# Kernel optimization log

Measured on AMD Instinct MI355X. Metric: run time of the kernel, lower is better.

The kernel has to match this reference:

```python
import jax, jax.numpy as jnp
import numpy as np

B, SQ, HIDDEN = 2, 2048, 2048
HEADS, GROUPS, KVC = 16, 4, 128
HPG = HEADS // GROUPS          # heads per group
LAYER_INDEX = 1
SCALE = KVC ** -0.5            # attention_softmax_scale_power = 0.5


def setup_inputs() -> dict:
    key = jax.random.key(0)
    k1, k2, k3, k4 = jax.random.split(key, 4)
    return {
        "x": jax.random.normal(k1, (B, SQ, HIDDEN), jnp.float32),
        "w_q": jax.random.normal(k2, (HIDDEN, HEADS * KVC), jnp.float32) * 0.02,
        "w_kv": jax.random.normal(k3, (HIDDEN, 2 * GROUPS * KVC), jnp.float32) * 0.02,
        "w_dense": jax.random.normal(k4, (HEADS * KVC, HIDDEN), jnp.float32) * 0.02,
    }


def reference(x, w_q, w_kv, w_dense):
    b, sq, _ = x.shape
    sk = sq
    # QKV projections
    q = jnp.einsum("bsh,he->bse", x, w_q).reshape(b, sq, GROUPS, HPG, KVC)
    kv = jnp.einsum("bsh,he->bse", x, w_kv)
    k, v = jnp.split(kv, 2, axis=-1)
    k = k.reshape(b, sk, GROUPS, KVC)
    v = v.reshape(b, sk, GROUPS, KVC)
    # scaled QK^T with the per-layer scale trick: alpha = scale/L in input
    # dtype, then cast to fp32 and multiply by L (as in _attn_fused)
    scores = jnp.einsum("bqgpd,bkgd->bgqpk", q, k) * (SCALE / LAYER_INDEX)
    scores = scores.astype(jnp.float32) * LAYER_INDEX
    # causal mask: mask = ~triu(ones, diagonal=1) -> keep where q_idx >= k_idx
    causal = (jnp.arange(sq)[:, None] >= jnp.arange(sk)[None, :])
    scores = jnp.where(causal[None, None, :, None, :], scores, -jnp.inf)
    probs = jax.nn.softmax(scores, axis=-1).astype(x.dtype)
    # dropout p = 0.0 -> no-op
    ctx = jnp.einsum("bgqpk,bkgd->bqgpd", probs, v).reshape(b, sq, HEADS * KVC)
    return jnp.einsum("bse,eh->bsh", ctx, w_dense)
```

## Files before the change

### kernel.cpp

```cpp
#include <hip/hip_runtime.h>
#include <hip/hip_bf16.h>


typedef __attribute__((ext_vector_type(4))) float f32x4;
typedef __attribute__((ext_vector_type(8))) short bf16x8;
typedef __attribute__((ext_vector_type(4))) short bf16x4;

__device__ __forceinline__ unsigned short f2bf(float f) {
    unsigned u = __builtin_bit_cast(unsigned, f);
    unsigned r = u + 0x7fffu + ((u >> 16) & 1u);
    return (unsigned short)(r >> 16);
}

__device__ __forceinline__ unsigned cvtpk_bf16(float lo, float hi) {
    unsigned r;
    asm("v_cvt_pk_bf16_f32 %0, %1, %2" : "=v"(r) : "v"(lo), "v"(hi));
    return r;
}

__device__ __forceinline__ void gl_lds16(const void* g, void* l) {
    __builtin_amdgcn_global_load_lds(
        (const __attribute__((address_space(1))) unsigned int*)g,
        (__attribute__((address_space(3))) unsigned int*)l, 16, 0, 0);
}

__global__ __launch_bounds__(256)
void xcvt_kernel(const float* __restrict__ in, unsigned short* __restrict__ out)
{
    size_t i = ((size_t)blockIdx.x * 256 + threadIdx.x) * 8;
    float4 a = *reinterpret_cast<const float4*>(&in[i]);
    float4 b = *reinterpret_cast<const float4*>(&in[i + 4]);
    bf16x8 o = { (short)f2bf(a.x), (short)f2bf(a.y),
                 (short)f2bf(a.z), (short)f2bf(a.w),
                 (short)f2bf(b.x), (short)f2bf(b.y),
                 (short)f2bf(b.z), (short)f2bf(b.w) };
    *reinterpret_cast<bf16x8*>(&out[i]) = o;
}

__global__ __launch_bounds__(256)
void wtrans_kernel(const float* __restrict__ in, unsigned short* __restrict__ out,
                   int K, int N)
{
    __shared__ unsigned short T[64][72];
    const int n0 = blockIdx.x * 64, k0 = blockIdx.y * 64;
    const int tid = threadIdx.x;
#pragma unroll
    for (int i = 0; i < 4; ++i) {
        int f = tid + i * 256;
        int r = f >> 4;
        int c4 = (f & 15) * 4;
        float4 v = *reinterpret_cast<const float4*>(&in[(size_t)(k0 + r) * N + n0 + c4]);
        bf16x4 pk = { (short)f2bf(v.x), (short)f2bf(v.y),
                      (short)f2bf(v.z), (short)f2bf(v.w) };
        *reinterpret_cast<bf16x4*>(&T[r][c4]) = pk;
    }
    __syncthreads();
#pragma unroll
    for (int i = 0; i < 2; ++i) {
        int f = tid + i * 256;
        int nn = f >> 3;
        int s8 = (f & 7) * 8;
        bf16x8 o;
#pragma unroll
        for (int j = 0; j < 8; ++j) o[j] = T[s8 + j][nn];
        *reinterpret_cast<bf16x8*>(&out[(size_t)(n0 + nn) * K + k0 + s8]) = o;
    }
}

template<bool SPLIT_QKV>
__global__ __launch_bounds__(256)
void gemm_bt_kernel(const unsigned short* __restrict__ A,
                    const unsigned short* __restrict__ BT,
                    void* __restrict__ C0v, void* __restrict__ C1v,
                    int M, int N, int K)
{
    __shared__ __align__(16) unsigned short Alds[2][128 * 64];
    __shared__ __align__(16) unsigned short Blds[2][128 * 64];

    const int tid = threadIdx.x;
    const int lane = tid & 63;
    const int wid = tid >> 6;
    const int wr = wid >> 1, wc = wid & 1;
    const int m0 = blockIdx.y * 128;
    const int n0 = blockIdx.x * 128;
    const int l16 = lane & 15, lg = lane >> 4;

    f32x4 acc[4][4];
#pragma unroll
    for (int m = 0; m < 4; ++m)
#pragma unroll
        for (int n = 0; n < 4; ++n) acc[m][n] = (f32x4){0.f, 0.f, 0.f, 0.f};

    auto stage = [&](int kt, int bi) {
#pragma unroll
        for (int i = 0; i < 4; ++i) {
            int row = i * 32 + (tid >> 3);
            int cb = ((tid & 7) * 16) ^ ((row & 7) << 4);
            gl_lds16((const char*)A + ((size_t)(m0 + row) * K + kt) * 2 + cb,
                     (char*)(&Alds[bi][0]) + i * 4096 + wid * 1024);
            gl_lds16((const char*)BT + ((size_t)(n0 + row) * K + kt) * 2 + cb,
                     (char*)(&Blds[bi][0]) + i * 4096 + wid * 1024);
        }
    };

    const int NK = K / 64;
    stage(0, 0);
    int cur = 0;

    for (int kti = 0; kti < NK; ++kti) {
        if (kti + 1 < NK) {
            stage((kti + 1) * 64, cur ^ 1);
            asm volatile("s_waitcnt vmcnt(8)" ::: "memory");
        } else {
            asm volatile("s_waitcnt vmcnt(0)" ::: "memory");
        }
        __builtin_amdgcn_s_barrier();

        const char* Ab = (const char*)(&Alds[cur][0]);
        const char* Bb = (const char*)(&Blds[cur][0]);

        bf16x8 af[2][4], bf[2][4];
#pragma unroll
        for (int kd = 0; kd < 2; ++kd) {
#pragma unroll
            for (int m = 0; m < 4; ++m) {
                int row = wr * 64 + m * 16 + l16;
                af[kd][m] = *reinterpret_cast<const bf16x8*>(
                    Ab + row * 128 + ((kd * 64 + lg * 16) ^ ((row & 7) << 4)));
            }
#pragma unroll
            for (int n = 0; n < 4; ++n) {
                int row = wc * 64 + n * 16 + l16;
                bf[kd][n] = *reinterpret_cast<const bf16x8*>(
                    Bb + row * 128 + ((kd * 64 + lg * 16) ^ ((row & 7) << 4)));
            }
        }
#pragma unroll
        for (int kd = 0; kd < 2; ++kd)
#pragma unroll
            for (int m = 0; m < 4; ++m)
#pragma unroll
                for (int n = 0; n < 4; ++n)
                    acc[m][n] = __builtin_amdgcn_mfma_f32_16x16x32_bf16(
                        af[kd][m], bf[kd][n], acc[m][n], 0, 0, 0);

        __builtin_amdgcn_s_barrier();
        cur ^= 1;
    }

#pragma unroll
    for (int m = 0; m < 4; ++m) {
#pragma unroll
        for (int n = 0; n < 4; ++n) {
#pragma unroll
            for (int r = 0; r < 4; ++r) {
                int row = m0 + wr * 64 + m * 16 + lg * 4 + r;
                int col = n0 + wc * 64 + n * 16 + l16;
                float val = acc[m][n][r];
                if constexpr (SPLIT_QKV) {
                    if (n0 < 2048)
                        ((unsigned short*)C0v)[(size_t)row * 2048 + col] =
                            f2bf(val * 0.12751879523209208f);
                    else
                        ((unsigned short*)C1v)[(size_t)row * 1024 + (col - 2048)] = f2bf(val);
                } else {
                    ((float*)C0v)[(size_t)row * N + col] = val;
                }
            }
        }
    }
}

__global__ __launch_bounds__(256)
void vtrans_kernel(const unsigned short* __restrict__ kv,
                   unsigned short* __restrict__ vt)
{
    __shared__ unsigned short T[64][140];
    const int bg = blockIdx.y;
    const int b = bg >> 2, g = bg & 3;
    const int s0 = blockIdx.x * 64;
    const int tid = threadIdx.x;

#pragma unroll
    for (int i = 0; i < 4; ++i) {
        int f = tid + i * 256;
        int sl = f >> 4;
        int d0 = (f & 15) * 8;
        bf16x8 v = *reinterpret_cast<const bf16x8*>(
            &kv[(size_t)(b * 2048 + s0 + sl) * 1024 + 512 + g * 128 + d0]);
        bf16x4 lo = { v[0], v[1], v[2], v[3] };
        bf16x4 hi = { v[4], v[5], v[6], v[7] };
        *reinterpret_cast<bf16x4*>(&T[sl][d0])     = lo;
        *reinterpret_cast<bf16x4*>(&T[sl][d0 + 4]) = hi;
    }
    __syncthreads();
#pragma unroll
    for (int i = 0; i < 4; ++i) {
        int f = tid + i * 256;
        int d = f >> 3;
        int s8 = (f & 7) * 8;
        bf16x8 o;
#pragma unroll
        for (int j = 0; j < 8; ++j) o[j] = T[s8 + j][d];
        *reinterpret_cast<bf16x8*>(
            &vt[(size_t)(bg * 128 + d) * 2048 + s0 + s8]) = o;
    }
}

__global__ __launch_bounds__(256)
void attn_kernel(const unsigned short* __restrict__ Q,
                 const unsigned short* __restrict__ KV,
                 const unsigned short* __restrict__ VT,
                 unsigned short* __restrict__ CTX)
{
    constexpr int SQ = 2048;
    __shared__ __align__(16) unsigned short Klds[64 * 128];
    __shared__ __align__(16) unsigned short Vlds[128 * 64];
    __shared__ __align__(16) unsigned short Pl[4][16][64];

    const int tid = threadIdx.x;
    const int lane = tid & 63;
    const int w = tid >> 6;
    const int l16 = lane & 15, lg = lane >> 4;

    const int bid = blockIdx.x;
    const int gb = bid & 7;
    const int g = gb & 3, b = gb >> 2;
    const int qt = 127 - (bid >> 3);
    const int hh = g * 4 + w;

    const size_t qbase = (size_t)b * SQ * 2048;
    const char* KVb = (const char*)KV + (size_t)b * SQ * 2048;
    const char* VTb = (const char*)VT;

    bf16x8 qfrag[4];
#pragma unroll
    for (int kd = 0; kd < 4; ++kd)
        qfrag[kd] = *reinterpret_cast<const bf16x8*>(
            &Q[qbase + (size_t)(qt * 16 + l16) * 2048 + hh * 128 + kd * 32 + lg * 8]);

    float lsum = 0.f;
    f32x4 acc[8];
#pragma unroll
    for (int nd = 0; nd < 8; ++nd) acc[nd] = (f32x4){0.f,0.f,0.f,0.f};

    const int ntiles = qt / 4 + 1;
    const int pswz = (l16 & 7) << 3;

    for (int t = 0; t < ntiles; ++t) {
        const int k0 = t * 64;
#pragma unroll
        for (int i = 0; i < 4; ++i) {
            int row = w * 16 + i * 4 + (lane >> 4);
            int scol = ((lane & 15) * 16) ^ ((row & 7) << 4);
            gl_lds16(KVb + (size_t)(k0 + row) * 2048 + g * 256 + scol,
                     (char*)Klds + w * 4096 + i * 1024);
        }
#pragma unroll
        for (int i = 0; i < 4; ++i) {
            int row = w * 32 + i * 8 + (lane >> 3);
            int scol = ((lane & 7) * 16) ^ ((row & 7) << 4);
            gl_lds16(VTb + ((size_t)(gb * 128 + row) * 2048 + k0) * 2 + scol,
                     (char*)Vlds + w * 4096 + i * 1024);
        }
        __syncthreads();

        f32x4 st[4];
#pragma unroll
        for (int nf = 0; nf < 4; ++nf) st[nf] = (f32x4){0.f,0.f,0.f,0.f};
        __builtin_amdgcn_s_setprio(1);
#pragma unroll
        for (int nf = 0; nf < 4; ++nf) {
            int row = nf * 16 + l16;
#pragma unroll
            for (int kd = 0; kd < 4; ++kd) {
                bf16x8 kf = *reinterpret_cast<const bf16x8*>(
                    (const char*)Klds + row * 256 +
                    ((kd * 64 + lg * 16) ^ ((row & 7) << 4)));
                st[nf] = __builtin_amdgcn_mfma_f32_16x16x32_bf16(
                    kf, qfrag[kd], st[nf], 0, 0, 0);
            }
        }
        __builtin_amdgcn_s_setprio(0);

        const bool diag = (t == ntiles - 1);
        {
            float lacc = 0.f;
            const int q = qt * 16 + l16;
#pragma unroll
            for (int nf = 0; nf < 4; ++nf) {
                float cs0 = st[nf][0];
                float cs1 = st[nf][1];
                float cs2 = st[nf][2];
                float cs3 = st[nf][3];
                if (diag) {
                    const int keyb = k0 + nf * 16 + lg * 4;
                    if (keyb + 0 > q) cs0 = -INFINITY;
                    if (keyb + 1 > q) cs1 = -INFINITY;
                    if (keyb + 2 > q) cs2 = -INFINITY;
                    if (keyb + 3 > q) cs3 = -INFINITY;
                }
                float p0 = exp2f(cs0), p1 = exp2f(cs1);
                float p2 = exp2f(cs2), p3 = exp2f(cs3);
                lacc += (p0 + p1) + (p2 + p3);
                uint2 pk = { cvtpk_bf16(p0, p1), cvtpk_bf16(p2, p3) };
                *reinterpret_cast<uint2*>(
                    &Pl[w][l16][(nf * 16 + lg * 4) ^ pswz]) = pk;
            }
            lacc += __shfl_xor(lacc, 16, 64);
            lacc += __shfl_xor(lacc, 32, 64);
            lsum += lacc;
        }

        __builtin_amdgcn_s_setprio(1);
#pragma unroll
        for (int kc = 0; kc < 2; ++kc) {
            bf16x8 pf = *reinterpret_cast<const bf16x8*>(
                &Pl[w][l16][(kc * 32 + lg * 8) ^ pswz]);
#pragma unroll
            for (int nd = 0; nd < 8; ++nd) {
                int row = nd * 16 + l16;
                bf16x8 vf = *reinterpret_cast<const bf16x8*>(
                    (const char*)Vlds + row * 128 +
                    ((kc * 64 + lg * 16) ^ ((row & 7) << 4)));
                acc[nd] = __builtin_amdgcn_mfma_f32_16x16x32_bf16(
                    vf, pf, acc[nd], 0, 0, 0);
            }
        }
        __builtin_amdgcn_s_setprio(0);
        __syncthreads();
    }

    {
        float inv = 1.0f / lsum;
        const int q = qt * 16 + l16;
#pragma unroll
        for (int nd = 0; nd < 8; ++nd) {
            bf16x4 o = { (short)f2bf(acc[nd][0] * inv),
                         (short)f2bf(acc[nd][1] * inv),
                         (short)f2bf(acc[nd][2] * inv),
                         (short)f2bf(acc[nd][3] * inv) };
            *reinterpret_cast<bf16x4*>(
                &CTX[qbase + (size_t)q * 2048 + hh * 128 + nd * 16 + lg * 4]) = o;
        }
    }
}

extern "C" void kernel_launch(void* const* d_in, const int* in_sizes, int n_in,
                              void* d_out, int out_size, void* d_ws, size_t ws_size,
                              hipStream_t stream)
{
    const float* x       = (const float*)d_in[0];
    const float* w_q     = (const float*)d_in[1];
    const float* w_kv    = (const float*)d_in[2];
    const float* w_dense = (const float*)d_in[3];

    const int M = 4096;

    char* ws = (char*)d_ws;
    unsigned short* kv_buf  = (unsigned short*)(ws);
    unsigned short* ctx_buf = (unsigned short*)(ws + (8u << 20));
    unsigned short* wqT     = (unsigned short*)(ws + (24u << 20));
    unsigned short* wkvT    = (unsigned short*)(ws + (32u << 20));
    unsigned short* wdT     = wqT;
    unsigned short* xbf    = (unsigned short*)d_out;
    unsigned short* q_buf  = (unsigned short*)d_out + (size_t)M * 2048;
    unsigned short* vt_buf = (unsigned short*)d_out;

    dim3 blk(256);
    xcvt_kernel<<<dim3(4096), blk, 0, stream>>>(x, xbf);
    wtrans_kernel<<<dim3(32, 32), blk, 0, stream>>>(w_q, wqT, 2048, 2048);
    wtrans_kernel<<<dim3(16, 32), blk, 0, stream>>>(w_kv, wkvT, 2048, 1024);
    gemm_bt_kernel<true><<<dim3(24, 32), blk, 0, stream>>>(
        xbf, wqT, (void*)q_buf, (void*)kv_buf, M, 3072, 2048);
    wtrans_kernel<<<dim3(32, 32), blk, 0, stream>>>(w_dense, wdT, 2048, 2048);
    vtrans_kernel<<<dim3(32, 8), blk, 0, stream>>>(kv_buf, vt_buf);
    attn_kernel<<<dim3(1024), blk, 0, stream>>>(q_buf, kv_buf, vt_buf, ctx_buf);
    gemm_bt_kernel<false><<<dim3(16, 32), blk, 0, stream>>>(
        ctx_buf, wdT, d_out, nullptr, M, 2048, 2048);
}
```

Before: 202.4 us.

## Switch GEMM to triple-buffered K=32 tiles with prefetch depth two

The GEMM main loop now uses K-tiles of 32 instead of 64 and keeps three LDS buffers, issuing global-to-LDS loads two iterations ahead instead of one. The LDS layout is repacked so two 32-wide rows share one 128-byte swizzled line, and the staging addresses are precomputed once per thread. The goal is to hide global memory latency better while using less LDS per block, which may allow more blocks per CU. In exchange there are twice as many barriers and loop iterations, each with half the MFMA work.

```diff
diff --git a/kernel.cpp b/kernel.cpp
--- a/kernel.cpp
+++ b/kernel.cpp
@@ -74,8 +74,8 @@
                     void* __restrict__ C0v, void* __restrict__ C1v,
                     int M, int N, int K)
 {
-    __shared__ __align__(16) unsigned short Alds[2][128 * 64];
-    __shared__ __align__(16) unsigned short Blds[2][128 * 64];
+    __shared__ __align__(16) unsigned short Alds[3][128 * 32];
+    __shared__ __align__(16) unsigned short Blds[3][128 * 32];
 
     const int tid = threadIdx.x;
     const int lane = tid & 63;
@@ -91,61 +91,69 @@
 #pragma unroll
         for (int n = 0; n < 4; ++n) acc[m][n] = (f32x4){0.f, 0.f, 0.f, 0.f};
 
+    int srow[2], skb[2];
+#pragma unroll
+    for (int i = 0; i < 2; ++i) {
+        int L = i * 4096 + tid * 16;
+        int R = L >> 7, c = L & 127;
+        int cp = c ^ ((R & 7) << 4);
+        srow[i] = 2 * R + (cp >> 6);
+        skb[i]  = cp & 63;
+    }
+
     auto stage = [&](int kt, int bi) {
 #pragma unroll
-        for (int i = 0; i < 4; ++i) {
-            int row = i * 32 + (tid >> 3);
-            int cb = ((tid & 7) * 16) ^ ((row & 7) << 4);
-            gl_lds16((const char*)A + ((size_t)(m0 + row) * K + kt) * 2 + cb,
-                     (char*)(&Alds[bi][0]) + i * 4096 + wid * 1024);
-            gl_lds16((const char*)BT + ((size_t)(n0 + row) * K + kt) * 2 + cb,
-                     (char*)(&Blds[bi][0]) + i * 4096 + wid * 1024);
+        for (int i = 0; i < 2; ++i) {
+            int L = i * 4096 + tid * 16;
+            gl_lds16((const char*)A + ((size_t)(m0 + srow[i]) * K + kt) * 2 + skb[i],
+                     (char*)(&Alds[bi][0]) + L);
+            gl_lds16((const char*)BT + ((size_t)(n0 + srow[i]) * K + kt) * 2 + skb[i],
+                     (char*)(&Blds[bi][0]) + L);
         }
     };
 
-    const int NK = K / 64;
+    const int NK = K / 32;
     stage(0, 0);
-    int cur = 0;
-
-    for (int kti = 0; kti < NK; ++kti) {
-        if (kti + 1 < NK) {
-            stage((kti + 1) * 64, cur ^ 1);
+    stage(32, 1);
+
+    for (int t = 0; t < NK; ++t) {
+        const int bi = t % 3;
+        if (t + 2 < NK) {
+            stage((t + 2) * 32, (t + 2) % 3);
             asm volatile("s_waitcnt vmcnt(8)" ::: "memory");
+        } else if (t + 1 < NK) {
+            asm volatile("s_waitcnt vmcnt(4)" ::: "memory");
         } else {
             asm volatile("s_waitcnt vmcnt(0)" ::: "memory");
         }
         __builtin_amdgcn_s_barrier();
 
-        const char* Ab = (const char*)(&Alds[cur][0]);
-        const char* Bb = (const char*)(&Blds[cur][0]);
-
-        bf16x8 af[2][4], bf[2][4];
-#pragma unroll
-        for (int kd = 0; kd < 2; ++kd) {
-#pragma unroll
-            for (int m = 0; m < 4; ++m) {
-                int row = wr * 64 + m * 16 + l16;
-                af[kd][m] = *reinterpret_cast<const bf16x8*>(
-                    Ab + row * 128 + ((kd * 64 + lg * 16) ^ ((row & 7) << 4)));
-            }
-#pragma unroll
-            for (int n = 0; n < 4; ++n) {
-                int row = wc * 64 + n * 16 + l16;
-                bf[kd][n] = *reinterpret_cast<const bf16x8*>(
-                    Bb + row * 128 + ((kd * 64 + lg * 16) ^ ((row & 7) << 4)));
-            }
-        }
-#pragma unroll
-        for (int kd = 0; kd < 2; ++kd)
-#pragma unroll
-            for (int m = 0; m < 4; ++m)
-#pragma unroll
-                for (int n = 0; n < 4; ++n)
-                    acc[m][n] = __builtin_amdgcn_mfma_f32_16x16x32_bf16(
-                        af[kd][m], bf[kd][n], acc[m][n], 0, 0, 0);
+        const char* Ab = (const char*)(&Alds[bi][0]);
+        const char* Bb = (const char*)(&Blds[bi][0]);
+
+        bf16x8 af[4], bf[4];
+#pragma unroll
+        for (int m = 0; m < 4; ++m) {
+            int row = wr * 64 + m * 16 + l16;
+            int byte = (row >> 1) * 128 +
+                       ((((row & 1) << 6) + lg * 16) ^ (((row >> 1) & 7) << 4));
+            af[m] = *reinterpret_cast<const bf16x8*>(Ab + byte);
+        }
+#pragma unroll
+        for (int n = 0; n < 4; ++n) {
+            int row = wc * 64 + n * 16 + l16;
+            int byte = (row >> 1) * 128 +
+                       ((((row & 1) << 6) + lg * 16) ^ (((row >> 1) & 7) << 4));
+            bf[n] = *reinterpret_cast<const bf16x8*>(Bb + byte);
+        }
+#pragma unroll
+        for (int m = 0; m < 4; ++m)
+#pragma unroll
+            for (int n = 0; n < 4; ++n)
+                acc[m][n] = __builtin_amdgcn_mfma_f32_16x16x32_bf16(
+                    af[m], bf[n], acc[m][n], 0, 0, 0);
 
         __builtin_amdgcn_s_barrier();
-        cur ^= 1;
     }
 
 #pragma unroll
```

After: 204.0 us. No clear change (+0.8%).

## Double-buffer K/V tiles and pair complementary causal query tiles per block

Applied to the files above, without the earlier changes.

The attention kernel now keeps two LDS buffers for K and V and prefetches the next key tile while computing on the current one, waiting with vmcnt and raw barriers instead of a full sync. Each block now processes two query tiles, qt=127-pi and qt=pi, so every block does the same amount of causal work, and the grid is halved to 512 blocks. This is meant to hide global-to-LDS load latency and remove the causal tail imbalance. In exchange the kernel uses twice the LDS, which may lower occupancy, and it launches half as many blocks.

```diff
diff --git a/kernel.cpp b/kernel.cpp
--- a/kernel.cpp
+++ b/kernel.cpp
@@ -214,8 +214,8 @@
                  unsigned short* __restrict__ CTX)
 {
     constexpr int SQ = 2048;
-    __shared__ __align__(16) unsigned short Klds[64 * 128];
-    __shared__ __align__(16) unsigned short Vlds[128 * 64];
+    __shared__ __align__(16) unsigned short Klds[2][64 * 128];
+    __shared__ __align__(16) unsigned short Vlds[2][128 * 64];
     __shared__ __align__(16) unsigned short Pl[4][16][64];
 
     const int tid = threadIdx.x;
@@ -226,122 +226,141 @@
     const int bid = blockIdx.x;
     const int gb = bid & 7;
     const int g = gb & 3, b = gb >> 2;
-    const int qt = 127 - (bid >> 3);
+    const int pi = bid >> 3;
     const int hh = g * 4 + w;
 
     const size_t qbase = (size_t)b * SQ * 2048;
     const char* KVb = (const char*)KV + (size_t)b * SQ * 2048;
     const char* VTb = (const char*)VT;
 
-    bf16x8 qfrag[4];
-#pragma unroll
-    for (int kd = 0; kd < 4; ++kd)
-        qfrag[kd] = *reinterpret_cast<const bf16x8*>(
-            &Q[qbase + (size_t)(qt * 16 + l16) * 2048 + hh * 128 + kd * 32 + lg * 8]);
-
-    float lsum = 0.f;
-    f32x4 acc[8];
-#pragma unroll
-    for (int nd = 0; nd < 8; ++nd) acc[nd] = (f32x4){0.f,0.f,0.f,0.f};
-
-    const int ntiles = qt / 4 + 1;
     const int pswz = (l16 & 7) << 3;
 
-    for (int t = 0; t < ntiles; ++t) {
+    auto stage = [&](int t, int bi) {
         const int k0 = t * 64;
 #pragma unroll
         for (int i = 0; i < 4; ++i) {
             int row = w * 16 + i * 4 + (lane >> 4);
             int scol = ((lane & 15) * 16) ^ ((row & 7) << 4);
             gl_lds16(KVb + (size_t)(k0 + row) * 2048 + g * 256 + scol,
-                     (char*)Klds + w * 4096 + i * 1024);
+                     (char*)(&Klds[bi][0]) + w * 4096 + i * 1024);
         }
 #pragma unroll
         for (int i = 0; i < 4; ++i) {
             int row = w * 32 + i * 8 + (lane >> 3);
             int scol = ((lane & 7) * 16) ^ ((row & 7) << 4);
             gl_lds16(VTb + ((size_t)(gb * 128 + row) * 2048 + k0) * 2 + scol,
-                     (char*)Vlds + w * 4096 + i * 1024);
-        }
-        __syncthreads();
-
-        f32x4 st[4];
-#pragma unroll
-        for (int nf = 0; nf < 4; ++nf) st[nf] = (f32x4){0.f,0.f,0.f,0.f};
-        __builtin_amdgcn_s_setprio(1);
-#pragma unroll
-        for (int nf = 0; nf < 4; ++nf) {
-            int row = nf * 16 + l16;
-#pragma unroll
-            for (int kd = 0; kd < 4; ++kd) {
-                bf16x8 kf = *reinterpret_cast<const bf16x8*>(
-                    (const char*)Klds + row * 256 +
-                    ((kd * 64 + lg * 16) ^ ((row & 7) << 4)));
-                st[nf] = __builtin_amdgcn_mfma_f32_16x16x32_bf16(
-                    kf, qfrag[kd], st[nf], 0, 0, 0);
-            }
-        }
-        __builtin_amdgcn_s_setprio(0);
-
-        const bool diag = (t == ntiles - 1);
+                     (char*)(&Vlds[bi][0]) + w * 4096 + i * 1024);
+        }
+    };
+
+#pragma unroll 1
+    for (int seg = 0; seg < 2; ++seg) {
+        const int qt = seg ? pi : (127 - pi);
+        const int ntiles = qt / 4 + 1;
+
+        bf16x8 qfrag[4];
+#pragma unroll
+        for (int kd = 0; kd < 4; ++kd)
+            qfrag[kd] = *reinterpret_cast<const bf16x8*>(
+                &Q[qbase + (size_t)(qt * 16 + l16) * 2048 + hh * 128 + kd * 32 + lg * 8]);
+
+        float lsum = 0.f;
+        f32x4 acc[8];
+#pragma unroll
+        for (int nd = 0; nd < 8; ++nd) acc[nd] = (f32x4){0.f,0.f,0.f,0.f};
+
+        stage(0, 0);
+
+        for (int t = 0; t < ntiles; ++t) {
+            const int bi = t & 1;
+            const int k0 = t * 64;
+            if (t + 1 < ntiles) {
+                stage(t + 1, bi ^ 1);
+                asm volatile("s_waitcnt vmcnt(8)" ::: "memory");
+            } else {
+                asm volatile("s_waitcnt vmcnt(0)" ::: "memory");
+            }
+            __builtin_amdgcn_s_barrier();
+
+            const char* Kb = (const char*)(&Klds[bi][0]);
+            const char* Vb = (const char*)(&Vlds[bi][0]);
+
+            f32x4 st[4];
+#pragma unroll
+            for (int nf = 0; nf < 4; ++nf) st[nf] = (f32x4){0.f,0.f,0.f,0.f};
+            __builtin_amdgcn_s_setprio(1);
+#pragma unroll
+            for (int nf = 0; nf < 4; ++nf) {
+                int row = nf * 16 + l16;
+#pragma unroll
+                for (int kd = 0; kd < 4; ++kd) {
+                    bf16x8 kf = *reinterpret_cast<const bf16x8*>(
+                        Kb + row * 256 + ((kd * 64 + lg * 16) ^ ((row & 7) << 4)));
+                    st[nf] = __builtin_amdgcn_mfma_f32_16x16x32_bf16(
+                        kf, qfrag[kd], st[nf], 0, 0, 0);
+                }
+            }
+            __builtin_amdgcn_s_setprio(0);
+
+            const bool diag = (t == ntiles - 1);
+            {
+                float lacc = 0.f;
+                const int q = qt * 16 + l16;
+#pragma unroll
+                for (int nf = 0; nf < 4; ++nf) {
+                    float cs0 = st[nf][0];
+                    float cs1 = st[nf][1];
+                    float cs2 = st[nf][2];
+                    float cs3 = st[nf][3];
+                    if (diag) {
+                        const int keyb = k0 + nf * 16 + lg * 4;
+                        if (keyb + 0 > q) cs0 = -INFINITY;
+                        if (keyb + 1 > q) cs1 = -INFINITY;
+                        if (keyb + 2 > q) cs2 = -INFINITY;
+                        if (keyb + 3 > q) cs3 = -INFINITY;
+                    }
+                    float p0 = exp2f(cs0), p1 = exp2f(cs1);
+                    float p2 = exp2f(cs2), p3 = exp2f(cs3);
+                    lacc += (p0 + p1) + (p2 + p3);
+                    uint2 pk = { cvtpk_bf16(p0, p1), cvtpk_bf16(p2, p3) };
+                    *reinterpret_cast<uint2*>(
+                        &Pl[w][l16][(nf * 16 + lg * 4) ^ pswz]) = pk;
+                }
+                lacc += __shfl_xor(lacc, 16, 64);
+                lacc += __shfl_xor(lacc, 32, 64);
+                lsum += lacc;
+            }
+
+            __builtin_amdgcn_s_setprio(1);
+#pragma unroll
+            for (int kc = 0; kc < 2; ++kc) {
+                bf16x8 pf = *reinterpret_cast<const bf16x8*>(
+                    &Pl[w][l16][(kc * 32 + lg * 8) ^ pswz]);
+#pragma unroll
+                for (int nd = 0; nd < 8; ++nd) {
+                    int row = nd * 16 + l16;
+                    bf16x8 vf = *reinterpret_cast<const bf16x8*>(
+                        Vb + row * 128 + ((kc * 64 + lg * 16) ^ ((row & 7) << 4)));
+                    acc[nd] = __builtin_amdgcn_mfma_f32_16x16x32_bf16(
+                        vf, pf, acc[nd], 0, 0, 0);
+                }
+            }
+            __builtin_amdgcn_s_setprio(0);
+            __builtin_amdgcn_s_barrier();
+        }
+
         {
-            float lacc = 0.f;
+            float inv = 1.0f / lsum;
             const int q = qt * 16 + l16;
 #pragma unroll
-            for (int nf = 0; nf < 4; ++nf) {
-                float cs0 = st[nf][0];
-                float cs1 = st[nf][1];
-                float cs2 = st[nf][2];
-                float cs3 = st[nf][3];
-                if (diag) {
-                    const int keyb = k0 + nf * 16 + lg * 4;
-                    if (keyb + 0 > q) cs0 = -INFINITY;
-                    if (keyb + 1 > q) cs1 = -INFINITY;
-                    if (keyb + 2 > q) cs2 = -INFINITY;
-                    if (keyb + 3 > q) cs3 = -INFINITY;
-                }
-                float p0 = exp2f(cs0), p1 = exp2f(cs1);
-                float p2 = exp2f(cs2), p3 = exp2f(cs3);
-                lacc += (p0 + p1) + (p2 + p3);
-                uint2 pk = { cvtpk_bf16(p0, p1), cvtpk_bf16(p2, p3) };
-                *reinterpret_cast<uint2*>(
-                    &Pl[w][l16][(nf * 16 + lg * 4) ^ pswz]) = pk;
-            }
-            lacc += __shfl_xor(lacc, 16, 64);
-            lacc += __shfl_xor(lacc, 32, 64);
-            lsum += lacc;
-        }
-
-        __builtin_amdgcn_s_setprio(1);
-#pragma unroll
-        for (int kc = 0; kc < 2; ++kc) {
-            bf16x8 pf = *reinterpret_cast<const bf16x8*>(
-                &Pl[w][l16][(kc * 32 + lg * 8) ^ pswz]);
-#pragma unroll
             for (int nd = 0; nd < 8; ++nd) {
-                int row = nd * 16 + l16;
-                bf16x8 vf = *reinterpret_cast<const bf16x8*>(
-                    (const char*)Vlds + row * 128 +
-                    ((kc * 64 + lg * 16) ^ ((row & 7) << 4)));
-                acc[nd] = __builtin_amdgcn_mfma_f32_16x16x32_bf16(
-                    vf, pf, acc[nd], 0, 0, 0);
-            }
-        }
-        __builtin_amdgcn_s_setprio(0);
-        __syncthreads();
-    }
-
-    {
-        float inv = 1.0f / lsum;
-        const int q = qt * 16 + l16;
-#pragma unroll
-        for (int nd = 0; nd < 8; ++nd) {
-            bf16x4 o = { (short)f2bf(acc[nd][0] * inv),
-                         (short)f2bf(acc[nd][1] * inv),
-                         (short)f2bf(acc[nd][2] * inv),
-                         (short)f2bf(acc[nd][3] * inv) };
-            *reinterpret_cast<bf16x4*>(
-                &CTX[qbase + (size_t)q * 2048 + hh * 128 + nd * 16 + lg * 4]) = o;
+                bf16x4 o = { (short)f2bf(acc[nd][0] * inv),
+                             (short)f2bf(acc[nd][1] * inv),
+                             (short)f2bf(acc[nd][2] * inv),
+                             (short)f2bf(acc[nd][3] * inv) };
+                *reinterpret_cast<bf16x4*>(
+                    &CTX[qbase + (size_t)q * 2048 + hh * 128 + nd * 16 + lg * 4]) = o;
+            }
         }
     }
 }
@@ -375,7 +394,7 @@
         xbf, wqT, (void*)q_buf, (void*)kv_buf, M, 3072, 2048);
     wtrans_kernel<<<dim3(32, 32), blk, 0, stream>>>(w_dense, wdT, 2048, 2048);
     vtrans_kernel<<<dim3(32, 8), blk, 0, stream>>>(kv_buf, vt_buf);
-    attn_kernel<<<dim3(1024), blk, 0, stream>>>(q_buf, kv_buf, vt_buf, ctx_buf);
+    attn_kernel<<<dim3(512), blk, 0, stream>>>(q_buf, kv_buf, vt_buf, ctx_buf);
     gemm_bt_kernel<false><<<dim3(16, 32), blk, 0, stream>>>(
         ctx_buf, wdT, d_out, nullptr, M, 2048, 2048);
 }
```

Result: faster. 198.3 us (-2.0%).
